# Kernel optimization log

Measured on AMD Instinct MI355X. Metric: run time of the kernel, lower is better.

## Reference

```python
import jax, jax.numpy as jnp
import numpy as np

B = 2
D_MODEL = 768
N_HEADS = 16
N_POINTS = 4
SHAPES = [(16, 16), (32, 32), (64, 64), (96, 96)]  # (H, W) per level; query = last level
EPS = 1e-6


def layernorm(x, g, b):
    m = jnp.mean(x, -1, keepdims=True)
    xc = x - m
    v = jnp.mean(xc * xc, -1, keepdims=True)
    return xc * jax.lax.rsqrt(v + EPS) * g + b


def _bilinear(vflat, H, W, px, py):
    # vflat: (B, h, H*W, D); px/py: (B, Lq, h, P) unnormalized pixel coords
    # Equivalent to F.grid_sample(align_corners=False, padding_mode='zeros').
    x0f = jnp.floor(px); y0f = jnp.floor(py)
    lx = px - x0f; ly = py - y0f
    x0 = x0f.astype(jnp.int32); y0 = y0f.astype(jnp.int32)

    def gather(xi, yi, w):
        valid = ((xi >= 0) & (xi < W) & (yi >= 0) & (yi < H)).astype(vflat.dtype)
        idx = jnp.clip(yi, 0, H - 1) * W + jnp.clip(xi, 0, W - 1)
        idx = jnp.transpose(idx, (0, 2, 1, 3))        # (B, h, Lq, P)
        wv = jnp.transpose(w * valid, (0, 2, 1, 3))   # (B, h, Lq, P)
        b_, h_, q_, p_ = idx.shape
        g = jnp.take_along_axis(vflat, idx.reshape(b_, h_, q_ * p_)[..., None], axis=2)
        return g.reshape(b_, h_, q_, p_, -1) * wv[..., None]

    return (gather(x0, y0, (1 - lx) * (1 - ly)) + gather(x0 + 1, y0, lx * (1 - ly))
            + gather(x0, y0 + 1, (1 - lx) * ly) + gather(x0 + 1, y0 + 1, lx * ly))


def ms_deform_attn(query, ref_pts, feat, shapes, Wv, bv, Woff, boff, Wa, ba, Wo, bo):
    # query: (B, Lq, C); ref_pts: (1, Lq, 1, 2) in [0,1]; feat: (B, Lin, C)
    Bq, Lq, C = query.shape
    L, h, P = len(shapes), N_HEADS, N_POINTS
    D = C // h
    value = (feat @ Wv + bv).reshape(Bq, -1, h, D)
    off = (query @ Woff + boff).reshape(Bq, Lq, h, L, P, 2)
    w = jax.nn.softmax((query @ Wa + ba).reshape(Bq, Lq, h, L * P), axis=-1)
    w = w.reshape(Bq, Lq, h, L, P)
    normalizer = jnp.array([[W_, H_] for (H_, W_) in shapes], dtype=query.dtype)  # (L, 2) = [W, H]
    loc = ref_pts[:, :, None, :, None, :] + off / normalizer[None, None, None, :, None, :]
    out = jnp.zeros((Bq, h, Lq, D), query.dtype)
    start = 0
    for l, (H_, W_) in enumerate(shapes):
        vl = jnp.transpose(value[:, start:start + H_ * W_], (0, 2, 1, 3))  # (B, h, HW, D)
        start += H_ * W_
        px = loc[:, :, :, l, :, 0] * W_ - 0.5
        py = loc[:, :, :, l, :, 1] * H_ - 0.5
        samp = _bilinear(vl, H_, W_, px, py)                   # (B, h, Lq, P, D)
        wl = jnp.transpose(w[:, :, :, l, :], (0, 2, 1, 3))     # (B, h, Lq, P)
        out = out + jnp.einsum('bhqpd,bhqp->bhqd', samp, wl)
    out = jnp.transpose(out, (0, 2, 1, 3)).reshape(Bq, Lq, C)
    return out @ Wo + bo


def ref_points(e, dtype=jnp.float32):
    # torch.linspace(0.5, e-0.5, e)/e == (arange(e)+0.5)/e
    lin = (jnp.arange(e, dtype=dtype) + 0.5) / e
    ry, rx = jnp.meshgrid(lin, lin, indexing='ij')
    return jnp.stack([rx.ravel(), ry.ravel()], -1)[None, :, None, :]  # (1, e*e, 1, 2)


def setup_inputs() -> dict:
    key = jax.random.key(0)
    ks = jax.random.split(key, 16)
    d, h, P = D_MODEL, N_HEADS, N_POINTS
    inp = {}
    for i, (name, (H_, W_)) in enumerate(zip(['src0', 'src1', 'src2', 'src3'], SHAPES)):
        inp[name] = jax.random.normal(ks[i], (B, H_ * W_, d), jnp.float32)
    for pre in ('qn', 'fn', 'n1'):
        inp[pre + '_g'] = jnp.ones((d,), jnp.float32)
        inp[pre + '_b'] = jnp.zeros((d,), jnp.float32)
    inp['gamma1'] = 0.1 * jnp.ones((d,), jnp.float32)
    inp['gamma2'] = 0.1 * jnp.ones((d,), jnp.float32)

    def lin(k, din, dout):
        return jax.random.normal(k, (din, dout), jnp.float32) * (din ** -0.5)

    inp['c_Wv'] = lin(ks[4], d, d);               inp['c_bv'] = jnp.zeros((d,), jnp.float32)
    inp['c_Woff'] = lin(ks[5], d, h * 4 * P * 2); inp['c_boff'] = jnp.zeros((h * 4 * P * 2,), jnp.float32)
    inp['c_Wa'] = lin(ks[6], d, h * 4 * P);       inp['c_ba'] = jnp.zeros((h * 4 * P,), jnp.float32)
    inp['c_Wo'] = lin(ks[7], d, d);               inp['c_bo'] = jnp.zeros((d,), jnp.float32)
    inp['s_Wv'] = lin(ks[8], d, d);               inp['s_bv'] = jnp.zeros((d,), jnp.float32)
    inp['s_Woff'] = lin(ks[9], d, h * P * 2);     inp['s_boff'] = jnp.zeros((h * P * 2,), jnp.float32)
    inp['s_Wa'] = lin(ks[10], d, h * P);          inp['s_ba'] = jnp.zeros((h * P,), jnp.float32)
    inp['s_Wo'] = lin(ks[11], d, d);              inp['s_bo'] = jnp.zeros((d,), jnp.float32)
    return inp


def reference(src0, src1, src2, src3, qn_g, qn_b, fn_g, fn_b, n1_g, n1_b,
              gamma1, gamma2,
              c_Wv, c_bv, c_Woff, c_boff, c_Wa, c_ba, c_Wo, c_bo,
              s_Wv, s_bv, s_Woff, s_boff, s_Wa, s_ba, s_Wo, s_bo):
    feat = jnp.concatenate([src0, src1, src2, src3], axis=1)
    query = src3  # query_layer = -1
    e = SHAPES[-1][0]
    ref = ref_points(e, query.dtype)
    attn = ms_deform_attn(layernorm(query, qn_g, qn_b), ref, layernorm(feat, fn_g, fn_b),
                          SHAPES, c_Wv, c_bv, c_Woff, c_boff, c_Wa, c_ba, c_Wo, c_bo)
    attn1 = layernorm(attn, n1_g, n1_b)
    attn2 = ms_deform_attn(attn1, ref, attn1, [SHAPES[-1]],
                           s_Wv, s_bv, s_Woff, s_boff, s_Wa, s_ba, s_Wo, s_bo)
    attn = attn + gamma2 * attn2
    return query + gamma1 * attn
```

## Files before the change

### kernel.cpp

```cpp
#include <hip/hip_runtime.h>
#include <stdint.h>

typedef unsigned short u16;
typedef __attribute__((ext_vector_type(8))) __bf16 bf16x8;
typedef __attribute__((ext_vector_type(4))) float f32x4;
typedef __attribute__((ext_vector_type(2))) float f32x2;
typedef __attribute__((ext_vector_type(8))) u16 u16x8;
typedef __attribute__((ext_vector_type(4))) u16 u16x4;

#define DEV __device__ __forceinline__

DEV u16 f2b(float f) {
  union { float f; uint32_t u; } v; v.f = f;
  uint32_t u = v.u;
  return (u16)((u + 0x7fffu + ((u >> 16) & 1u)) >> 16);
}
DEV float b2f(u16 h) {
  union { uint32_t u; float f; } v; v.u = ((uint32_t)h) << 16;
  return v.f;
}
DEV float u2f(uint32_t u) {
  union { uint32_t u; float f; } v; v.u = u;
  return v.f;
}
DEV uint8_t f2fp8(float f) {
  return (uint8_t)(__builtin_amdgcn_cvt_pk_fp8_f32(f, f, 0, false) & 0xff);
}
DEV void fma8f8(f32x2* acc, uint2 v, float w) {
  f32x2 wv = {w, w};
  f32x2 x0 = __builtin_amdgcn_cvt_pk_f32_fp8(v.x, false);
  f32x2 x1 = __builtin_amdgcn_cvt_pk_f32_fp8(v.x, true);
  f32x2 x2 = __builtin_amdgcn_cvt_pk_f32_fp8(v.y, false);
  f32x2 x3 = __builtin_amdgcn_cvt_pk_f32_fp8(v.y, true);
  acc[0] += wv * x0;
  acc[1] += wv * x1;
  acc[2] += wv * x2;
  acc[3] += wv * x3;
}

__global__ __launch_bounds__(256) void wconv_kernel(
    const float* __restrict__ W0, const float* __restrict__ W1,
    const float* __restrict__ W2, const float* __restrict__ W3,
    const float* __restrict__ W4, const float* __restrict__ W5,
    const float* __restrict__ W6, const float* __restrict__ W7,
    u16* __restrict__ dst) {
  __shared__ float s[32][33];
  int bx = blockIdx.x;
  int ct = bx / 24;
  int kt = bx - ct * 24;
  const float* Wsrc; int N; int rowbase; int c0;
  if (ct < 24)       { Wsrc = W0; N = 768; rowbase = 0;    c0 = ct; }
  else if (ct < 40)  { Wsrc = W1; N = 512; rowbase = 768;  c0 = ct - 24; }
  else if (ct < 48)  { Wsrc = W2; N = 256; rowbase = 1280; c0 = ct - 40; }
  else if (ct < 72)  { Wsrc = W3; N = 768; rowbase = 1536; c0 = ct - 48; }
  else if (ct < 96)  { Wsrc = W4; N = 768; rowbase = 2304; c0 = ct - 72; }
  else if (ct < 100) { Wsrc = W5; N = 128; rowbase = 3072; c0 = ct - 96; }
  else if (ct < 104) { Wsrc = W6; N = 64;  rowbase = 3200; c0 = ct - 100; }
  else               { Wsrc = W7; N = 768; rowbase = 3328; c0 = ct - 104; }
  const int tx = threadIdx.x & 31, ty = threadIdx.x >> 5;
  const int n = c0 * 32 + tx;
  const int k0 = kt * 32;
  #pragma unroll
  for (int j = 0; j < 4; ++j) {
    int k = k0 + ty + j * 8;
    s[ty + j * 8][tx] = (n < N) ? Wsrc[(size_t)k * N + n] : 0.0f;
  }
  __syncthreads();
  #pragma unroll
  for (int j = 0; j < 4; ++j) {
    int nr = c0 * 32 + ty + j * 8;
    dst[(size_t)(rowbase + nr) * 768 + k0 + tx] = f2b(s[tx][ty + j * 8]);
  }
}

DEV void ln_core(float4 v, const float* __restrict__ g, const float* __restrict__ b,
                 u16* __restrict__ o, int t, float* red) {
  float s = v.x + v.y + v.z + v.w;
  float s2 = v.x * v.x + v.y * v.y + v.z * v.z + v.w * v.w;
  #pragma unroll
  for (int m = 1; m < 64; m <<= 1) { s += __shfl_xor(s, m); s2 += __shfl_xor(s2, m); }
  if ((t & 63) == 0) { red[t >> 6] = s; red[3 + (t >> 6)] = s2; }
  __syncthreads();
  float S = red[0] + red[1] + red[2];
  float S2 = red[3] + red[4] + red[5];
  float mean = S * (1.0f / 768.0f);
  float var = S2 * (1.0f / 768.0f) - mean * mean;
  float rstd = rsqrtf(var + 1e-6f);
  float4 gv = ((const float4*)g)[t], bv = ((const float4*)b)[t];
  u16x4 ov;
  ov[0] = f2b((v.x - mean) * rstd * gv.x + bv.x);
  ov[1] = f2b((v.y - mean) * rstd * gv.y + bv.y);
  ov[2] = f2b((v.z - mean) * rstd * gv.z + bv.z);
  ov[3] = f2b((v.w - mean) * rstd * gv.w + bv.w);
  *(u16x4*)(o + t * 4) = ov;
}

__global__ __launch_bounds__(192) void ln_rows_kernel(const float* __restrict__ in,
    const float* __restrict__ g, const float* __restrict__ b, u16* __restrict__ out) {
  __shared__ float red[6];
  size_t row = blockIdx.x;
  int t = threadIdx.x;
  ln_core(((const float4*)(in + row * 768))[t], g, b, out + row * 768, t, red);
}

__global__ __launch_bounds__(192) void ln_rows_b16_kernel(const u16* __restrict__ in,
    const float* __restrict__ g, const float* __restrict__ b, u16* __restrict__ out) {
  __shared__ float red[6];
  size_t row = blockIdx.x;
  int t = threadIdx.x;
  u16x4 r = *(const u16x4*)(in + row * 768 + t * 4);
  float4 v = {b2f(r[0]), b2f(r[1]), b2f(r[2]), b2f(r[3])};
  ln_core(v, g, b, out + row * 768, t, red);
}

__global__ __launch_bounds__(192) void ln_feat_kernel(const float* __restrict__ s0,
    const float* __restrict__ s1, const float* __restrict__ s2, const float* __restrict__ s3,
    const float* __restrict__ g, const float* __restrict__ b, u16* __restrict__ out) {
  __shared__ float red[6];
  int row = blockIdx.x;
  int bb = row / 14592, pos = row - bb * 14592;
  const float* x;
  if (pos < 256)       x = s0 + ((size_t)bb * 256  + pos) * 768;
  else if (pos < 1280) x = s1 + ((size_t)bb * 1024 + (pos - 256)) * 768;
  else if (pos < 5376) x = s2 + ((size_t)bb * 4096 + (pos - 1280)) * 768;
  else                 x = s3 + ((size_t)bb * 9216 + (pos - 5376)) * 768;
  int t = threadIdx.x;
  ln_core(((const float4*)x)[t], g, b, out + (size_t)row * 768, t, red);
}

enum { MODE_F32 = 0, MODE_BF16 = 1, MODE_FINAL = 2, MODE_FP8T = 3 };

template <int MODE, int NT, int LROW = 1>
__global__ __launch_bounds__(256) void gemm_kernel(
    const u16* __restrict__ A, const u16* __restrict__ Wt,
    const float* __restrict__ bias1, const float* __restrict__ bias2,
    int split, int nb, void* __restrict__ Cout, int N,
    const u16* __restrict__ attnb, const float* __restrict__ resid,
    const float* __restrict__ g1, const float* __restrict__ g2) {
  constexpr int K = 768;
  __shared__ u16 smem[4 * 128 * 64];
  const int t = threadIdx.x;
  const int lane = t & 63;
  const int w = t >> 6;
  const int wr = w >> 1, wc = w & 1;
  const int chunk = gridDim.x >> 3;
  const int tile = (blockIdx.x & 7) * chunk + (blockIdx.x >> 3);
  const int tm = tile / NT, tn = tile - tm * NT;
  const size_t m0 = (size_t)tm * 128;
  const int n0 = tn * 128;

  f32x4 acc[4][4] = {};

  auto STAGE = [&](int buf, int kt) {
    u16* sA = smem + buf * 16384;
    u16* sB = sA + 8192;
    #pragma unroll
    for (int i = 0; i < 4; ++i) {
      int ci = i * 256 + t;
      int row = ci >> 3, c8 = ci & 7;
      int kc = c8 ^ (row & 7);
      const u16* ga = A + (m0 + row) * K + kt + kc * 8;
      const u16* gb = Wt + ((size_t)n0 + row) * K + kt + kc * 8;
      __builtin_amdgcn_global_load_lds((const __attribute__((address_space(1))) void*)ga,
          (__attribute__((address_space(3))) void*)(sA + ci * 8), 16, 0, 0);
      __builtin_amdgcn_global_load_lds((const __attribute__((address_space(1))) void*)gb,
          (__attribute__((address_space(3))) void*)(sB + ci * 8), 16, 0, 0);
    }
  };

  STAGE(0, 0);
  __syncthreads();
  int cur = 0;
  for (int kt = 0; kt < K; kt += 64) {
    if (kt + 64 < K) STAGE(cur ^ 1, kt + 64);
    const u16* sA = smem + cur * 16384;
    const u16* sB = sA + 8192;
    #pragma unroll
    for (int ks = 0; ks < 2; ++ks) {
      bf16x8 af[4], bfr[4];
      #pragma unroll
      for (int m = 0; m < 4; ++m) {
        int row = wr * 64 + m * 16 + (lane & 15);
        int pc = (ks * 4 + (lane >> 4)) ^ (row & 7);
        af[m] = *(const bf16x8*)(sA + row * 64 + pc * 8);
      }
      #pragma unroll
      for (int n = 0; n < 4; ++n) {
        int row = wc * 64 + n * 16 + (lane & 15);
        int pc = (ks * 4 + (lane >> 4)) ^ (row & 7);
        bfr[n] = *(const bf16x8*)(sB + row * 64 + pc * 8);
      }
      #pragma unroll
      for (int m = 0; m < 4; ++m)
        #pragma unroll
        for (int n = 0; n < 4; ++n)
          acc[m][n] = __builtin_amdgcn_mfma_f32_16x16x32_bf16(af[m], bfr[n], acc[m][n], 0, 0, 0);
    }
    __syncthreads();
    cur ^= 1;
  }

  if constexpr (MODE == MODE_BF16) {
    #pragma unroll
    for (int m = 0; m < 4; ++m) {
      #pragma unroll
      for (int n = 0; n < 4; ++n) {
        int lcol = wc * 64 + n * 16 + (lane & 15);
        int gcol = n0 + lcol;
        float bv = (gcol < split) ? bias1[gcol] : ((gcol < nb) ? bias2[gcol - split] : 0.0f);
        #pragma unroll
        for (int r = 0; r < 4; ++r) {
          int lrow = wr * 64 + m * 16 + (lane >> 4) * 4 + r;
          smem[lrow * 136 + lcol] = f2b(acc[m][n][r] + bv);
        }
      }
    }
    __syncthreads();
    #pragma unroll
    for (int i = 0; i < 8; ++i) {
      int c = t + 256 * i;
      int lrow = c >> 4, col8 = (c & 15) * 8;
      u16x8 vv = *(const u16x8*)(smem + lrow * 136 + col8);
      int gcol = n0 + col8;
      size_t grow = m0 + (size_t)lrow;
      *(u16x8*)((u16*)Cout + grow * (size_t)N + gcol) = vv;
    }
  } else if constexpr (MODE == MODE_FP8T) {
    uint8_t* s8 = (uint8_t*)smem;
    #pragma unroll
    for (int m = 0; m < 4; ++m) {
      #pragma unroll
      for (int n = 0; n < 4; ++n) {
        int lcol = wc * 64 + n * 16 + (lane & 15);
        int gcol = n0 + lcol;
        float bv = (gcol < split) ? bias1[gcol] : ((gcol < nb) ? bias2[gcol - split] : 0.0f);
        #pragma unroll
        for (int r = 0; r < 4; ++r) {
          int lrow = wr * 64 + m * 16 + (lane >> 4) * 4 + r;
          s8[lrow * 144 + lcol] = f2fp8(acc[m][n][r] + bv);
        }
      }
    }
    __syncthreads();
    #pragma unroll
    for (int i = 0; i < 4; ++i) {
      int c = t + 256 * i;
      int lrow = c >> 3, col16 = (c & 7) * 16;
      uint4 vv = *(const uint4*)(s8 + lrow * 144 + col16);
      int gcol = n0 + col16;
      size_t grow = m0 + (size_t)lrow;
      int gi = (int)grow;
      int bb = gi / LROW, pos = gi - bb * LROW;
      int hh = gcol / 48, dd = gcol - hh * 48;
      *(uint4*)((uint8_t*)Cout + (((size_t)bb * 16 + hh) * LROW + pos) * 48 + dd) = vv;
    }
  } else {
    #pragma unroll
    for (int m = 0; m < 4; ++m) {
      #pragma unroll
      for (int n = 0; n < 4; ++n) {
        int col = n0 + wc * 64 + n * 16 + (lane & 15);
        float bv = (col < split) ? bias1[col] : ((col < nb) ? bias2[col - split] : 0.0f);
        #pragma unroll
        for (int r = 0; r < 4; ++r) {
          size_t grow = m0 + (size_t)(wr * 64 + m * 16 + (lane >> 4) * 4 + r);
          float v = acc[m][n][r] + bv;
          size_t idx = grow * (size_t)N + col;
          if constexpr (MODE == MODE_F32) {
            ((float*)Cout)[idx] = v;
          } else {
            ((float*)Cout)[idx] = resid[idx] + g1[col] * (b2f(attnb[idx]) + g2[col] * v);
          }
        }
      }
    }
  }
}

#define GATHER4F8(ga, gb, gc, gd, ii) \
  uint2 ga = *(const uint2*)(vB + ((ii).x + hd)); \
  uint2 gb = *(const uint2*)(vB + ((ii).y + hd)); \
  uint2 gc = *(const uint2*)(vB + ((ii).z + hd)); \
  uint2 gd = *(const uint2*)(vB + ((ii).w + hd));
#define FMA4F8(ga, gb, gc, gd, ww) \
  fma8f8(acc0, ga, (ww).x); fma8f8(acc1, gb, (ww).y); \
  fma8f8(acc0, gc, (ww).z); fma8f8(acc1, gd, (ww).w);

__global__ __launch_bounds__(192, 4) void samp_c_kernel(const uint8_t* __restrict__ value,
    const u16* __restrict__ offa, u16* __restrict__ out) {
  __shared__ uint8_t sdesc[2 * 16 * 528];
  const int orig = blockIdx.x;
  const int cpx = gridDim.x >> 3;
  const int bq0 = ((orig & 7) * cpx + (orig >> 3)) * 2;
  const int t = threadIdx.x;

  if (t < 128) {
    const int qi = t >> 6, h = (t >> 2) & 15, l = t & 3;
    const int bq = bq0 + qi;
    const int b = bq / 9216, q = bq - b * 9216;
    const u16* rw = offa + (size_t)bq * 768;
    u16x8 A0 = *(const u16x8*)(rw + 512 + h * 16);
    u16x8 A1 = *(const u16x8*)(rw + 512 + h * 16 + 8);
    float lg[16];
    #pragma unroll
    for (int i = 0; i < 8; ++i) { lg[i] = b2f(A0[i]); lg[8 + i] = b2f(A1[i]); }
    float mx = lg[0];
    #pragma unroll
    for (int i = 1; i < 16; ++i) mx = fmaxf(mx, lg[i]);
    float sum = 0.0f;
    #pragma unroll
    for (int i = 0; i < 16; ++i) sum += __expf(lg[i] - mx);
    const float rs = 1.0f / sum;
    float w0 = (l == 0) ? lg[0] : ((l == 1) ? lg[4] : ((l == 2) ? lg[8]  : lg[12]));
    float w1 = (l == 0) ? lg[1] : ((l == 1) ? lg[5] : ((l == 2) ? lg[9]  : lg[13]));
    float w2 = (l == 0) ? lg[2] : ((l == 1) ? lg[6] : ((l == 2) ? lg[10] : lg[14]));
    float w3 = (l == 0) ? lg[3] : ((l == 1) ? lg[7] : ((l == 2) ? lg[11] : lg[15]));

    const int Wd = (l == 3) ? 96 : (16 << l);
    const int STl = (l == 0) ? 0 : ((l == 1) ? 256 : ((l == 2) ? 1280 : 5376));
    const float fW = (float)Wd;
    const float rx = ((q % 96) + 0.5f) * (1.0f / 96.0f);
    const float ry = ((q / 96) + 0.5f) * (1.0f / 96.0f);
    const int headbase = (b * 16 + h) * 14592 + STl;

    u16x8 O = *(const u16x8*)(rw + h * 32 + l * 8);
    float oxs[4] = {b2f(O[0]), b2f(O[2]), b2f(O[4]), b2f(O[6])};
    float oys[4] = {b2f(O[1]), b2f(O[3]), b2f(O[5]), b2f(O[7])};
    float wgs[4] = {w0, w1, w2, w3};
    uint8_t* dpb = sdesc + (qi * 16 + h) * 528 + l * 32;
    #pragma unroll
    for (int pt = 0; pt < 4; ++pt) {
      float px = rx * fW + oxs[pt] - 0.5f;
      float py = ry * fW + oys[pt] - 0.5f;
      float wgt = __expf(wgs[pt] - mx) * rs;
      float x0f = floorf(px), y0f = floorf(py);
      float lx = px - x0f, ly = py - y0f;
      int x0 = (int)x0f, y0 = (int)y0f;
      int xc0 = min(max(x0, 0), Wd - 1), xc1 = min(max(x0 + 1, 0), Wd - 1);
      int yc0 = min(max(y0, 0), Wd - 1), yc1 = min(max(y0 + 1, 0), Wd - 1);
      float wx0 = ((unsigned)x0       < (unsigned)Wd) ? (1.0f - lx) : 0.0f;
      float wx1 = ((unsigned)(x0 + 1) < (unsigned)Wd) ? lx          : 0.0f;
      float wy0 = (((unsigned)y0       < (unsigned)Wd) ? (1.0f - ly) : 0.0f) * wgt;
      float wy1 = (((unsigned)(y0 + 1) < (unsigned)Wd) ? ly          : 0.0f) * wgt;
      int4 ii;
      ii.x = (headbase + yc0 * Wd + xc0) * 48;
      ii.y = (headbase + yc0 * Wd + xc1) * 48;
      ii.z = (headbase + yc1 * Wd + xc0) * 48;
      ii.w = (headbase + yc1 * Wd + xc1) * 48;
      float4 ww = {wx0 * wy0, wx1 * wy0, wx0 * wy1, wx1 * wy1};
      *(int4*)(dpb + pt * 128) = ii;
      *(float4*)(dpb + pt * 128 + 16) = ww;
    }
  }
  __syncthreads();

  const int qi = t / 96, r = t - qi * 96;
  const int h = r / 6, d8 = r - h * 6;
  const int bq = bq0 + qi;
  const int hd = d8 * 8;
  const uint8_t* vB = value;
  const uint8_t* dp = sdesc + (qi * 16 + h) * 528;

  f32x2 acc0[4] = {}, acc1[4] = {};
  #pragma unroll
  for (int pb = 0; pb < 4; ++pb) {
    const uint8_t* dpp = dp + pb * 128;
    int4   i0 = *(const int4*)(dpp);
    float4 w0 = *(const float4*)(dpp + 16);
    int4   i1 = *(const int4*)(dpp + 32);
    float4 w1 = *(const float4*)(dpp + 48);
    int4   i2 = *(const int4*)(dpp + 64);
    float4 w2 = *(const float4*)(dpp + 80);
    int4   i3 = *(const int4*)(dpp + 96);
    float4 w3 = *(const float4*)(dpp + 112);
    GATHER4F8(g00, g01, g02, g03, i0)
    GATHER4F8(g10, g11, g12, g13, i1)
    GATHER4F8(g20, g21, g22, g23, i2)
    GATHER4F8(g30, g31, g32, g33, i3)
    FMA4F8(g00, g01, g02, g03, w0)
    FMA4F8(g10, g11, g12, g13, w1)
    FMA4F8(g20, g21, g22, g23, w2)
    FMA4F8(g30, g31, g32, g33, w3)
  }
  u16x8 o;
  #pragma unroll
  for (int j = 0; j < 4; ++j) {
    o[2*j]   = f2b(acc0[j][0] + acc1[j][0]);
    o[2*j+1] = f2b(acc0[j][1] + acc1[j][1]);
  }
  *(u16x8*)(out + (size_t)bq * 768 + h * 48 + d8 * 8) = o;
}

__global__ __launch_bounds__(192, 4) void samp_s_kernel(const uint8_t* __restrict__ value,
    const u16* __restrict__ offa, u16* __restrict__ out) {
  __shared__ uint8_t sdesc[2 * 16 * 144];
  const int orig = blockIdx.x;
  const int cpx = gridDim.x >> 3;
  const int bq0 = ((orig & 7) * cpx + (orig >> 3)) * 2;
  const int t = threadIdx.x;

  if (t < 32) {
    const int qi = t >> 4, h = t & 15;
    const int bq = bq0 + qi;
    const int b = bq / 9216, q = bq - b * 9216;
    const u16* rw = offa + (size_t)bq * 256;
    u16x4 Lv = *(const u16x4*)(rw + 128 + h * 4);
    float lg[4] = {b2f(Lv[0]), b2f(Lv[1]), b2f(Lv[2]), b2f(Lv[3])};
    float mx = fmaxf(fmaxf(lg[0], lg[1]), fmaxf(lg[2], lg[3]));
    float sum = __expf(lg[0] - mx) + __expf(lg[1] - mx) + __expf(lg[2] - mx) + __expf(lg[3] - mx);
    const float rs = 1.0f / sum;
    const float rx = ((q % 96) + 0.5f) * (1.0f / 96.0f);
    const float ry = ((q / 96) + 0.5f) * (1.0f / 96.0f);
    const int headbase = (b * 16 + h) * 9216;
    u16x8 O = *(const u16x8*)(rw + h * 8);
    float oxs[4] = {b2f(O[0]), b2f(O[2]), b2f(O[4]), b2f(O[6])};
    float oys[4] = {b2f(O[1]), b2f(O[3]), b2f(O[5]), b2f(O[7])};
    uint8_t* dpb = sdesc + (qi * 16 + h) * 144;
    #pragma unroll
    for (int pt = 0; pt < 4; ++pt) {
      float px = rx * 96.0f + oxs[pt] - 0.5f;
      float py = ry * 96.0f + oys[pt] - 0.5f;
      float wgt = __expf(lg[pt] - mx) * rs;
      float x0f = floorf(px), y0f = floorf(py);
      float lx = px - x0f, ly = py - y0f;
      int x0 = (int)x0f, y0 = (int)y0f;
      int xc0 = min(max(x0, 0), 95), xc1 = min(max(x0 + 1, 0), 95);
      int yc0 = min(max(y0, 0), 95), yc1 = min(max(y0 + 1, 0), 95);
      float wx0 = ((unsigned)x0       < 96u) ? (1.0f - lx) : 0.0f;
      float wx1 = ((unsigned)(x0 + 1) < 96u) ? lx          : 0.0f;
      float wy0 = (((unsigned)y0       < 96u) ? (1.0f - ly) : 0.0f) * wgt;
      float wy1 = (((unsigned)(y0 + 1) < 96u) ? ly          : 0.0f) * wgt;
      int4 ii;
      ii.x = (headbase + yc0 * 96 + xc0) * 48;
      ii.y = (headbase + yc0 * 96 + xc1) * 48;
      ii.z = (headbase + yc1 * 96 + xc0) * 48;
      ii.w = (headbase + yc1 * 96 + xc1) * 48;
      float4 ww = {wx0 * wy0, wx1 * wy0, wx0 * wy1, wx1 * wy1};
      *(int4*)(dpb + pt * 32) = ii;
      *(float4*)(dpb + pt * 32 + 16) = ww;
    }
  }
  __syncthreads();

  const int qi = t / 96, r = t - qi * 96;
  const int h = r / 6, d8 = r - h * 6;
  const int bq = bq0 + qi;
  const int hd = d8 * 8;
  const uint8_t* vB = value;
  const uint8_t* dp = sdesc + (qi * 16 + h) * 144;

  f32x2 acc0[4] = {}, acc1[4] = {};
  {
    int4   i0 = *(const int4*)(dp);
    float4 w0 = *(const float4*)(dp + 16);
    int4   i1 = *(const int4*)(dp + 32);
    float4 w1 = *(const float4*)(dp + 48);
    int4   i2 = *(const int4*)(dp + 64);
    float4 w2 = *(const float4*)(dp + 80);
    int4   i3 = *(const int4*)(dp + 96);
    float4 w3 = *(const float4*)(dp + 112);
    GATHER4F8(g00, g01, g02, g03, i0)
    GATHER4F8(g10, g11, g12, g13, i1)
    GATHER4F8(g20, g21, g22, g23, i2)
    GATHER4F8(g30, g31, g32, g33, i3)
    FMA4F8(g00, g01, g02, g03, w0)
    FMA4F8(g10, g11, g12, g13, w1)
    FMA4F8(g20, g21, g22, g23, w2)
    FMA4F8(g30, g31, g32, g33, w3)
  }
  u16x8 o;
  #pragma unroll
  for (int j = 0; j < 4; ++j) {
    o[2*j]   = f2b(acc0[j][0] + acc1[j][0]);
    o[2*j+1] = f2b(acc0[j][1] + acc1[j][1]);
  }
  *(u16x8*)(out + (size_t)bq * 768 + h * 48 + d8 * 8) = o;
}

extern "C" void kernel_launch(void* const* d_in, const int* in_sizes, int n_in,
                              void* d_out, int out_size, void* d_ws, size_t ws_size,
                              hipStream_t stream) {
  (void)in_sizes; (void)n_in; (void)out_size; (void)ws_size;
  const float* src0 = (const float*)d_in[0];
  const float* src1 = (const float*)d_in[1];
  const float* src2 = (const float*)d_in[2];
  const float* src3 = (const float*)d_in[3];
  const float* qn_g = (const float*)d_in[4];
  const float* qn_b = (const float*)d_in[5];
  const float* fn_g = (const float*)d_in[6];
  const float* fn_b = (const float*)d_in[7];
  const float* n1_g = (const float*)d_in[8];
  const float* n1_b = (const float*)d_in[9];
  const float* gamma1 = (const float*)d_in[10];
  const float* gamma2 = (const float*)d_in[11];
  const float* c_Wv  = (const float*)d_in[12]; const float* c_bv   = (const float*)d_in[13];
  const float* c_Woff= (const float*)d_in[14]; const float* c_boff = (const float*)d_in[15];
  const float* c_Wa  = (const float*)d_in[16]; const float* c_ba   = (const float*)d_in[17];
  const float* c_Wo  = (const float*)d_in[18]; const float* c_bo   = (const float*)d_in[19];
  const float* s_Wv  = (const float*)d_in[20]; const float* s_bv   = (const float*)d_in[21];
  const float* s_Woff= (const float*)d_in[22]; const float* s_boff = (const float*)d_in[23];
  const float* s_Wa  = (const float*)d_in[24]; const float* s_ba   = (const float*)d_in[25];
  const float* s_Wo  = (const float*)d_in[26]; const float* s_bo   = (const float*)d_in[27];

  constexpr int Lq = 9216;
  constexpr int Mq = 2 * Lq;
  constexpr int Mf = 2 * 14592;

  constexpr size_t O_qln   = 8u << 20;
  constexpr size_t O_fln   = O_qln   + (size_t)Mq * 768 * 2;
  constexpr size_t O_valc  = O_fln   + (size_t)Mf * 768 * 2;
  constexpr size_t O_offac = O_valc  + (size_t)Mf * 768;
  constexpr size_t O_sampc = O_qln;
  constexpr size_t O_attn  = O_fln;
  constexpr size_t O_attn1 = O_attn  + (size_t)Mq * 768 * 2;
  constexpr size_t O_vals  = O_attn1 + (size_t)Mq * 768 * 2;
  constexpr size_t O_offas = O_vals  + (size_t)Mq * 768;
  constexpr size_t O_samps = O_offas + (size_t)Mq * 256 * 2;

  uint8_t* ws = (uint8_t*)d_ws;
  u16* Wbase = (u16*)ws;
  auto Wrow = [&](int r) { return Wbase + (size_t)r * 768; };
  auto Wp = [&](size_t o) { return (u16*)(ws + o); };

  wconv_kernel<<<3072, 256, 0, stream>>>(c_Wv, c_Woff, c_Wa, c_Wo, s_Wv, s_Woff, s_Wa, s_Wo, Wbase);

  ln_rows_kernel<<<Mq, 192, 0, stream>>>(src3, qn_g, qn_b, Wp(O_qln));
  ln_feat_kernel<<<Mf, 192, 0, stream>>>(src0, src1, src2, src3, fn_g, fn_b, Wp(O_fln));

  gemm_kernel<MODE_FP8T, 6, 14592><<<(Mf / 128) * 6, 256, 0, stream>>>(
      Wp(O_fln), Wrow(0), c_bv, nullptr, 768, 768, ws + O_valc, 768,
      nullptr, nullptr, nullptr, nullptr);
  gemm_kernel<MODE_BF16, 6><<<(Mq / 128) * 6, 256, 0, stream>>>(
      Wp(O_qln), Wrow(768), c_boff, c_ba, 512, 768, Wp(O_offac), 768,
      nullptr, nullptr, nullptr, nullptr);

  samp_c_kernel<<<Mq / 2, 192, 0, stream>>>(ws + O_valc, Wp(O_offac), Wp(O_sampc));

  gemm_kernel<MODE_BF16, 6><<<(Mq / 128) * 6, 256, 0, stream>>>(
      Wp(O_sampc), Wrow(1536), c_bo, nullptr, 768, 768, Wp(O_attn), 768,
      nullptr, nullptr, nullptr, nullptr);

  ln_rows_b16_kernel<<<Mq, 192, 0, stream>>>(Wp(O_attn), n1_g, n1_b, Wp(O_attn1));

  gemm_kernel<MODE_FP8T, 6, 9216><<<(Mq / 128) * 6, 256, 0, stream>>>(
      Wp(O_attn1), Wrow(2304), s_bv, nullptr, 768, 768, ws + O_vals, 768,
      nullptr, nullptr, nullptr, nullptr);
  gemm_kernel<MODE_BF16, 2><<<(Mq / 128) * 2, 256, 0, stream>>>(
      Wp(O_attn1), Wrow(3072), s_boff, s_ba, 128, 192, Wp(O_offas), 256,
      nullptr, nullptr, nullptr, nullptr);

  samp_s_kernel<<<Mq / 2, 192, 0, stream>>>(ws + O_vals, Wp(O_offas), Wp(O_samps));

  gemm_kernel<MODE_FINAL, 6><<<(Mq / 128) * 6, 256, 0, stream>>>(
      Wp(O_samps), Wrow(3328), s_bo, nullptr, 768, 768, (float*)d_out, 768,
      Wp(O_attn), src3, gamma1, gamma2);
}
```

Before: 341.6 us.

## Widen sampling gathers to 16 FP8 channels and process four queries per block

Both deformable sampling kernels now have each thread gather 16 FP8 channels per corner with 128-bit loads instead of 8 with 64-bit loads. Each block now handles four queries with 256 threads, so all threads build sampling descriptors and 192 then do the gathers. This halves the number of gather instructions and gives more memory-level parallelism per load. In exchange each thread uses more accumulator registers and does more serial work, so latency hiding and occupancy may drop.

```diff
diff --git a/kernel.cpp b/kernel.cpp
--- a/kernel.cpp
+++ b/kernel.cpp
@@ -26,16 +26,16 @@
 DEV uint8_t f2fp8(float f) {
   return (uint8_t)(__builtin_amdgcn_cvt_pk_fp8_f32(f, f, 0, false) & 0xff);
 }
-DEV void fma8f8(f32x2* acc, uint2 v, float w) {
+DEV void fma16f8(f32x2* acc, uint4 v, float w) {
   f32x2 wv = {w, w};
-  f32x2 x0 = __builtin_amdgcn_cvt_pk_f32_fp8(v.x, false);
-  f32x2 x1 = __builtin_amdgcn_cvt_pk_f32_fp8(v.x, true);
-  f32x2 x2 = __builtin_amdgcn_cvt_pk_f32_fp8(v.y, false);
-  f32x2 x3 = __builtin_amdgcn_cvt_pk_f32_fp8(v.y, true);
-  acc[0] += wv * x0;
-  acc[1] += wv * x1;
-  acc[2] += wv * x2;
-  acc[3] += wv * x3;
+  const uint32_t* pv = (const uint32_t*)&v;
+  #pragma unroll
+  for (int j = 0; j < 4; ++j) {
+    f32x2 lo = __builtin_amdgcn_cvt_pk_f32_fp8(pv[j], false);
+    f32x2 hi = __builtin_amdgcn_cvt_pk_f32_fp8(pv[j], true);
+    acc[2 * j]     += wv * lo;
+    acc[2 * j + 1] += wv * hi;
+  }
 }
 
 __global__ __launch_bounds__(256) void wconv_kernel(
@@ -277,24 +277,15 @@
   }
 }
 
-#define GATHER4F8(ga, gb, gc, gd, ii) \
-  uint2 ga = *(const uint2*)(vB + ((ii).x + hd)); \
-  uint2 gb = *(const uint2*)(vB + ((ii).y + hd)); \
-  uint2 gc = *(const uint2*)(vB + ((ii).z + hd)); \
-  uint2 gd = *(const uint2*)(vB + ((ii).w + hd));
-#define FMA4F8(ga, gb, gc, gd, ww) \
-  fma8f8(acc0, ga, (ww).x); fma8f8(acc1, gb, (ww).y); \
-  fma8f8(acc0, gc, (ww).z); fma8f8(acc1, gd, (ww).w);
-
-__global__ __launch_bounds__(192, 4) void samp_c_kernel(const uint8_t* __restrict__ value,
+__global__ __launch_bounds__(256, 4) void samp_c_kernel(const uint8_t* __restrict__ value,
     const u16* __restrict__ offa, u16* __restrict__ out) {
-  __shared__ uint8_t sdesc[2 * 16 * 528];
+  __shared__ uint8_t sdesc[4 * 16 * 528];
   const int orig = blockIdx.x;
   const int cpx = gridDim.x >> 3;
-  const int bq0 = ((orig & 7) * cpx + (orig >> 3)) * 2;
+  const int bq0 = ((orig & 7) * cpx + (orig >> 3)) * 4;
   const int t = threadIdx.x;
 
-  if (t < 128) {
+  {
     const int qi = t >> 6, h = (t >> 2) & 15, l = t & 3;
     const int bq = bq0 + qi;
     const int b = bq / 9216, q = bq - b * 9216;
@@ -353,53 +344,52 @@
     }
   }
   __syncthreads();
-
-  const int qi = t / 96, r = t - qi * 96;
-  const int h = r / 6, d8 = r - h * 6;
+  if (t >= 192) return;
+
+  const int qi = t / 48, r = t - qi * 48;
+  const int h = r / 3, d16 = r - h * 3;
   const int bq = bq0 + qi;
-  const int hd = d8 * 8;
+  const int hd = d16 * 16;
   const uint8_t* vB = value;
   const uint8_t* dp = sdesc + (qi * 16 + h) * 528;
 
-  f32x2 acc0[4] = {}, acc1[4] = {};
-  #pragma unroll
-  for (int pb = 0; pb < 4; ++pb) {
-    const uint8_t* dpp = dp + pb * 128;
-    int4   i0 = *(const int4*)(dpp);
-    float4 w0 = *(const float4*)(dpp + 16);
-    int4   i1 = *(const int4*)(dpp + 32);
-    float4 w1 = *(const float4*)(dpp + 48);
-    int4   i2 = *(const int4*)(dpp + 64);
-    float4 w2 = *(const float4*)(dpp + 80);
-    int4   i3 = *(const int4*)(dpp + 96);
-    float4 w3 = *(const float4*)(dpp + 112);
-    GATHER4F8(g00, g01, g02, g03, i0)
-    GATHER4F8(g10, g11, g12, g13, i1)
-    GATHER4F8(g20, g21, g22, g23, i2)
-    GATHER4F8(g30, g31, g32, g33, i3)
-    FMA4F8(g00, g01, g02, g03, w0)
-    FMA4F8(g10, g11, g12, g13, w1)
-    FMA4F8(g20, g21, g22, g23, w2)
-    FMA4F8(g30, g31, g32, g33, w3)
-  }
-  u16x8 o;
+  f32x2 acc0[8] = {}, acc1[8] = {};
+  #pragma unroll
+  for (int p = 0; p < 16; ++p) {
+    const uint8_t* dpp = dp + p * 32;
+    int4   ii = *(const int4*)(dpp);
+    float4 ww = *(const float4*)(dpp + 16);
+    uint4 g0 = *(const uint4*)(vB + (ii.x + hd));
+    uint4 g1 = *(const uint4*)(vB + (ii.y + hd));
+    uint4 g2 = *(const uint4*)(vB + (ii.z + hd));
+    uint4 g3 = *(const uint4*)(vB + (ii.w + hd));
+    fma16f8(acc0, g0, ww.x);
+    fma16f8(acc1, g1, ww.y);
+    fma16f8(acc0, g2, ww.z);
+    fma16f8(acc1, g3, ww.w);
+  }
+  u16x8 o0, o1;
   #pragma unroll
   for (int j = 0; j < 4; ++j) {
-    o[2*j]   = f2b(acc0[j][0] + acc1[j][0]);
-    o[2*j+1] = f2b(acc0[j][1] + acc1[j][1]);
-  }
-  *(u16x8*)(out + (size_t)bq * 768 + h * 48 + d8 * 8) = o;
-}
-
-__global__ __launch_bounds__(192, 4) void samp_s_kernel(const uint8_t* __restrict__ value,
+    o0[2*j]   = f2b(acc0[j][0] + acc1[j][0]);
+    o0[2*j+1] = f2b(acc0[j][1] + acc1[j][1]);
+    o1[2*j]   = f2b(acc0[4+j][0] + acc1[4+j][0]);
+    o1[2*j+1] = f2b(acc0[4+j][1] + acc1[4+j][1]);
+  }
+  u16* op = out + (size_t)bq * 768 + h * 48 + d16 * 16;
+  *(u16x8*)op = o0;
+  *(u16x8*)(op + 8) = o1;
+}
+
+__global__ __launch_bounds__(256, 4) void samp_s_kernel(const uint8_t* __restrict__ value,
     const u16* __restrict__ offa, u16* __restrict__ out) {
-  __shared__ uint8_t sdesc[2 * 16 * 144];
+  __shared__ uint8_t sdesc[4 * 16 * 144];
   const int orig = blockIdx.x;
   const int cpx = gridDim.x >> 3;
-  const int bq0 = ((orig & 7) * cpx + (orig >> 3)) * 2;
+  const int bq0 = ((orig & 7) * cpx + (orig >> 3)) * 4;
   const int t = threadIdx.x;
 
-  if (t < 32) {
+  if (t < 64) {
     const int qi = t >> 4, h = t & 15;
     const int bq = bq0 + qi;
     const int b = bq / 9216, q = bq - b * 9216;
@@ -441,40 +431,41 @@
     }
   }
   __syncthreads();
-
-  const int qi = t / 96, r = t - qi * 96;
-  const int h = r / 6, d8 = r - h * 6;
+  if (t >= 192) return;
+
+  const int qi = t / 48, r = t - qi * 48;
+  const int h = r / 3, d16 = r - h * 3;
   const int bq = bq0 + qi;
-  const int hd = d8 * 8;
+  const int hd = d16 * 16;
   const uint8_t* vB = value;
   const uint8_t* dp = sdesc + (qi * 16 + h) * 144;
 
-  f32x2 acc0[4] = {}, acc1[4] = {};
-  {
-    int4   i0 = *(const int4*)(dp);
-    float4 w0 = *(const float4*)(dp + 16);
-    int4   i1 = *(const int4*)(dp + 32);
-    float4 w1 = *(const float4*)(dp + 48);
-    int4   i2 = *(const int4*)(dp + 64);
-    float4 w2 = *(const float4*)(dp + 80);
-    int4   i3 = *(const int4*)(dp + 96);
-    float4 w3 = *(const float4*)(dp + 112);
-    GATHER4F8(g00, g01, g02, g03, i0)
-    GATHER4F8(g10, g11, g12, g13, i1)
-    GATHER4F8(g20, g21, g22, g23, i2)
-    GATHER4F8(g30, g31, g32, g33, i3)
-    FMA4F8(g00, g01, g02, g03, w0)
-    FMA4F8(g10, g11, g12, g13, w1)
-    FMA4F8(g20, g21, g22, g23, w2)
-    FMA4F8(g30, g31, g32, g33, w3)
-  }
-  u16x8 o;
+  f32x2 acc0[8] = {}, acc1[8] = {};
+  #pragma unroll
+  for (int p = 0; p < 4; ++p) {
+    const uint8_t* dpp = dp + p * 32;
+    int4   ii = *(const int4*)(dpp);
+    float4 ww = *(const float4*)(dpp + 16);
+    uint4 g0 = *(const uint4*)(vB + (ii.x + hd));
+    uint4 g1 = *(const uint4*)(vB + (ii.y + hd));
+    uint4 g2 = *(const uint4*)(vB + (ii.z + hd));
+    uint4 g3 = *(const uint4*)(vB + (ii.w + hd));
+    fma16f8(acc0, g0, ww.x);
+    fma16f8(acc1, g1, ww.y);
+    fma16f8(acc0, g2, ww.z);
+    fma16f8(acc1, g3, ww.w);
+  }
+  u16x8 o0, o1;
   #pragma unroll
   for (int j = 0; j < 4; ++j) {
-    o[2*j]   = f2b(acc0[j][0] + acc1[j][0]);
-    o[2*j+1] = f2b(acc0[j][1] + acc1[j][1]);
-  }
-  *(u16x8*)(out + (size_t)bq * 768 + h * 48 + d8 * 8) = o;
+    o0[2*j]   = f2b(acc0[j][0] + acc1[j][0]);
+    o0[2*j+1] = f2b(acc0[j][1] + acc1[j][1]);
+    o1[2*j]   = f2b(acc0[4+j][0] + acc1[4+j][0]);
+    o1[2*j+1] = f2b(acc0[4+j][1] + acc1[4+j][1]);
+  }
+  u16* op = out + (size_t)bq * 768 + h * 48 + d16 * 16;
+  *(u16x8*)op = o0;
+  *(u16x8*)(op + 8) = o1;
 }
 
 extern "C" void kernel_launch(void* const* d_in, const int* in_sizes, int n_in,
@@ -534,7 +525,7 @@
       Wp(O_qln), Wrow(768), c_boff, c_ba, 512, 768, Wp(O_offac), 768,
       nullptr, nullptr, nullptr, nullptr);
 
-  samp_c_kernel<<<Mq / 2, 192, 0, stream>>>(ws + O_valc, Wp(O_offac), Wp(O_sampc));
+  samp_c_kernel<<<Mq / 4, 256, 0, stream>>>(ws + O_valc, Wp(O_offac), Wp(O_sampc));
 
   gemm_kernel<MODE_BF16, 6><<<(Mq / 128) * 6, 256, 0, stream>>>(
       Wp(O_sampc), Wrow(1536), c_bo, nullptr, 768, 768, Wp(O_attn), 768,
@@ -549,7 +540,7 @@
       Wp(O_attn1), Wrow(3072), s_boff, s_ba, 128, 192, Wp(O_offas), 256,
       nullptr, nullptr, nullptr, nullptr);
 
-  samp_s_kernel<<<Mq / 2, 192, 0, stream>>>(ws + O_vals, Wp(O_offas), Wp(O_samps));
+  samp_s_kernel<<<Mq / 4, 256, 0, stream>>>(ws + O_vals, Wp(O_offas), Wp(O_samps));
 
   gemm_kernel<MODE_FINAL, 6><<<(Mq / 128) * 6, 256, 0, stream>>>(
       Wp(O_samps), Wrow(3328), s_bo, nullptr, 768, 768, (float*)d_out, 768,
```

After: 333.8 us. 1.02x faster.
